# Kernel optimization log

Hardware: AMD Instinct MI355X
Metric: run time of the kernel (lower is better)

## Reference

```python
import jax, jax.numpy as jnp
import numpy as np

B, S, HID = 1, 2048, 2048
H = 16
DN, DR, DV = 128, 64, 128          # qk_nope_head_dim, qk_rope_head_dim, v_head_dim
DQ = DN + DR                        # q_head_dim = 192
QLR, KVLR = 1536, 512               # q_lora_rank, kv_lora_rank
MAXP = 32 * 1024
SCALE = DQ ** -0.5
EPS = 1e-6


def rmsnorm(x, w):
    return x * jax.lax.rsqrt(jnp.mean(x * x, axis=-1, keepdims=True) + EPS) * w


def rotate_half(x):
    h = x.shape[-1] // 2
    return jnp.concatenate((-x[..., h:], x[..., :h]), axis=-1)


def interleave_to_half(x):
    # torch: view(b,h,s,d//2,2).transpose(4,3).reshape(b,h,s,d)
    b, h, s, d = x.shape
    return x.reshape(b, h, s, d // 2, 2).transpose(0, 1, 2, 4, 3).reshape(b, h, s, d)


def setup_inputs() -> dict:
    key = jax.random.key(0)
    ks = jax.random.split(key, 8)
    def w(k, shape):
        fan_in = shape[-1]
        return jax.random.normal(k, shape, jnp.float32) * (fan_in ** -0.5)
    inp = {
        "hidden_states": jax.random.normal(ks[0], (B, S, HID), jnp.float32),
        "q_a_w": w(ks[1], (QLR, HID)),
        "q_a_ln": jnp.ones((QLR,), jnp.float32),
        "q_b_w": w(ks[2], (H * DQ, QLR)),
        "kv_a_w": w(ks[3], (KVLR + DR, HID)),
        "kv_a_ln": jnp.ones((KVLR,), jnp.float32),
        "kv_b_w": w(ks[4], (H * (DN + DV), KVLR)),
        "o_w": w(ks[5], (HID, H * DV)),
    }
    # rotary tables, seq_len = 32k
    inv_freq = 1.0 / (10000.0 ** (np.arange(0, DR, 2, dtype=np.float32) / DR))
    t = np.arange(MAXP, dtype=np.float32)
    freqs = np.outer(t, inv_freq)
    emb = np.concatenate((freqs, freqs), axis=-1)
    inp["cos"] = jnp.asarray(np.cos(emb), jnp.float32)
    inp["sin"] = jnp.asarray(np.sin(emb), jnp.float32)
    # bool mask, True = masked (causal)
    inp["attention_mask"] = jnp.triu(jnp.ones((S, S), bool), 1)[None, None]
    inp["position_ids"] = jnp.arange(S, dtype=jnp.int64 if jax.config.jax_enable_x64 else jnp.int32)[None].repeat(B, 0)
    return inp


def reference(hidden_states, q_a_w, q_a_ln, q_b_w, kv_a_w, kv_a_ln, kv_b_w, o_w,
              cos, sin, attention_mask, position_ids):
    b, s, _ = hidden_states.shape
    # low-rank Q: q_b(LN(q_a(x)))
    q = rmsnorm(hidden_states @ q_a_w.T, q_a_ln) @ q_b_w.T         # [b,s,H*DQ]
    q = q.reshape(b, s, H, DQ).transpose(0, 2, 1, 3)               # [b,H,s,DQ]
    q_nope, q_pe = q[..., :DN], q[..., DN:]
    # compressed KV + decoupled rope key
    ckv = hidden_states @ kv_a_w.T                                  # [b,s,KVLR+DR]
    compressed_kv, k_pe = ckv[..., :KVLR], ckv[..., KVLR:]
    k_pe = k_pe.reshape(b, s, 1, DR).transpose(0, 2, 1, 3)          # [b,1,s,DR]
    kv = rmsnorm(compressed_kv, kv_a_ln) @ kv_b_w.T                 # [b,s,H*(DN+DV)]
    kv = kv.reshape(b, s, H, DN + DV).transpose(0, 2, 1, 3)         # [b,H,s,DN+DV]
    k_nope, value_states = kv[..., :DN], kv[..., DN:]
    # rotary with interleaved->half reorder on the rope slice only
    cos_p = cos[position_ids][:, None]                              # [b,1,s,DR]
    sin_p = sin[position_ids][:, None]
    q_pe = interleave_to_half(q_pe)
    k_pe = interleave_to_half(k_pe)
    q_pe = q_pe * cos_p + rotate_half(q_pe) * sin_p
    k_pe = k_pe * cos_p + rotate_half(k_pe) * sin_p
    query_states = jnp.concatenate((q_nope, q_pe), axis=-1)         # [b,H,s,DQ]
    key_states = jnp.concatenate(
        (k_nope, jnp.broadcast_to(k_pe, (b, H, s, DR))), axis=-1)   # [b,H,s,DQ]
    # manual attention
    scores = jnp.einsum("bhqd,bhkd->bhqk", query_states, key_states) * SCALE
    scores = jnp.where(attention_mask, jnp.float32(-10000.0), scores)
    attn = jax.nn.softmax(scores.astype(jnp.float32), axis=-1).astype(query_states.dtype)
    attn_out = jnp.einsum("bhqk,bhkd->bhqd", attn, value_states)    # [b,H,s,DV]
    attn_out = attn_out.transpose(0, 2, 1, 3).reshape(b, s, H * DV)
    return attn_out @ o_w.T                                         # [b,s,HID]
```

## Files before the change

kernel.cpp:

```cpp
#include <hip/hip_runtime.h>
#include <stdint.h>

typedef unsigned short u16;
typedef __attribute__((ext_vector_type(8))) short short8;
typedef __attribute__((ext_vector_type(4))) float f32x4;
typedef __attribute__((ext_vector_type(4))) unsigned short ushort4_t;
typedef __attribute__((ext_vector_type(4))) float float4_t;

#define DEV_INLINE __device__ __forceinline__

DEV_INLINE u16 f2bf(float f) {
    union { float f; unsigned u; } x; x.f = f;
    unsigned u = x.u;
    unsigned r = (u + 0x7FFFu + ((u >> 16) & 1u)) >> 16;
    return (u16)r;
}

DEV_INLINE float bf2f(u16 b) {
    union { unsigned u; float f; } x; x.u = ((unsigned)b) << 16;
    return x.f;
}

DEV_INLINE float fexp2(float x) {
    float r;
    asm("v_exp_f32 %0, %1" : "=v"(r) : "v"(x));
    return r;
}

DEV_INLINE unsigned cvtpk_bf16(float lo, float hi) {
    unsigned r;
    asm("v_cvt_pk_bf16_f32 %0, %1, %2" : "=v"(r) : "v"(lo), "v"(hi));
    return r;
}

template <int CTRL>
DEV_INLINE float dppmaxf(float x) {
    union { float f; int i; } u; u.f = x;
    int y = __builtin_amdgcn_update_dpp(u.i, u.i, CTRL, 0xf, 0xf, true);
    union { int i; float f; } v; v.i = y;
    return fmaxf(x, v.f);
}

DEV_INLINE float dpp_xor1(float x) {
    union { float f; int i; } u; u.f = x;
    int y = __builtin_amdgcn_update_dpp(u.i, u.i, 0xB1, 0xf, 0xf, true);
    union { int i; float f; } v; v.i = y;
    return v.f;
}

DEV_INLINE float rmax16(float x) {
    x = dppmaxf<0xB1>(x);
    x = dppmaxf<0x4E>(x);
    x = dppmaxf<0x141>(x);
    x = dppmaxf<0x140>(x);
    return x;
}

__global__ void conv_multi(const float* __restrict__ s0, u16* __restrict__ d0, long e0,
                           const float* __restrict__ s1, u16* __restrict__ d1, long e1,
                           const float* __restrict__ s2, u16* __restrict__ d2, long e2,
                           const float* __restrict__ s3, u16* __restrict__ d3, long e3,
                           const float* __restrict__ s4, u16* __restrict__ d4, long e4) {
    long i = (long)blockIdx.x * 256 + threadIdx.x;
    const float* s; u16* d; long base;
    if      (i < e0) { s = s0; d = d0; base = 0; }
    else if (i < e1) { s = s1; d = d1; base = e0; }
    else if (i < e2) { s = s2; d = d2; base = e1; }
    else if (i < e3) { s = s3; d = d3; base = e2; }
    else if (i < e4) { s = s4; d = d4; base = e3; }
    else return;
    long j = i - base;
    float4_t v = ((const float4_t*)s)[j];
    ushort4_t o;
    o.x = f2bf(v.x); o.y = f2bf(v.y); o.z = f2bf(v.z); o.w = f2bf(v.w);
    ((ushort4_t*)d)[j] = o;
}

__global__ void conv_pad(const float* __restrict__ in, u16* __restrict__ out,
                         int rows_valid, long n4, int cols4) {
    long i = (long)blockIdx.x * blockDim.x + threadIdx.x;
    if (i >= n4) return;
    long row = i / cols4;
    ushort4_t o; o.x = 0; o.y = 0; o.z = 0; o.w = 0;
    if (row < rows_valid) {
        float4_t v = ((const float4_t*)in)[i];
        o.x = f2bf(v.x); o.y = f2bf(v.y); o.z = f2bf(v.z); o.w = f2bf(v.w);
    }
    ((ushort4_t*)out)[i] = o;
}

#define BK 32

DEV_INLINE void gload16(const u16* g, u16* l) {
    __builtin_amdgcn_global_load_lds((const __attribute__((address_space(1))) unsigned int*)g,
                                     (__attribute__((address_space(3))) unsigned int*)l,
                                     16, 0, 0);
}

template <typename OT>
__global__ __launch_bounds__(256) void gemm64_db(const u16* __restrict__ A, const u16* __restrict__ B,
                                                 OT* __restrict__ C, int M, int N, int K) {
    __shared__ u16 As[2][64 * BK];
    __shared__ u16 Bs[2][128 * BK];
    const int tid = threadIdx.x;
    const int wid = tid >> 6, lane = tid & 63;
    const int lm = lane & 15, lk = lane >> 4;
    const long bm = (long)blockIdx.y * 64, bn = (long)blockIdx.x * 128;

    f32x4 acc[4][2] = {};

    const int rowS = lane >> 2;
    const int colS = ((lane & 3) ^ ((lane >> 3) & 3)) * 8;
    const int cs = (lm >> 1) & 3;
    const u16* Ag = A + (bm + wid * 16 + rowS) * (long)K + colS;
    const u16* Bg = B + (bn + wid * 32 + rowS) * (long)K + colS;
    const int aoff = wid * 16 * BK;
    const int boff = wid * 32 * BK;

    gload16(Ag, &As[0][aoff]);
    gload16(Bg, &Bs[0][boff]);
    gload16(Bg + 16 * (long)K, &Bs[0][boff + 16 * BK]);
    __syncthreads();

    int cur = 0;
    for (int k0 = 0; k0 < K; k0 += BK) {
        if (k0 + BK < K) {
            gload16(Ag + k0 + BK, &As[cur ^ 1][aoff]);
            gload16(Bg + k0 + BK, &Bs[cur ^ 1][boff]);
            gload16(Bg + 16 * (long)K + k0 + BK, &Bs[cur ^ 1][boff + 16 * BK]);
        }
        short8 af[4], bfr[2];
#pragma unroll
        for (int m = 0; m < 4; ++m)
            af[m] = *(const short8*)&As[cur][(m * 16 + lm) * BK + (lk ^ cs) * 8];
#pragma unroll
        for (int n = 0; n < 2; ++n)
            bfr[n] = *(const short8*)&Bs[cur][(wid * 32 + n * 16 + lm) * BK + (lk ^ cs) * 8];
#pragma unroll
        for (int m = 0; m < 4; ++m)
#pragma unroll
            for (int n = 0; n < 2; ++n)
                acc[m][n] = __builtin_amdgcn_mfma_f32_16x16x32_bf16(af[m], bfr[n], acc[m][n], 0, 0, 0);
        __syncthreads();
        cur ^= 1;
    }

#pragma unroll
    for (int m = 0; m < 4; ++m)
#pragma unroll
        for (int n = 0; n < 2; ++n)
#pragma unroll
            for (int r = 0; r < 4; ++r) {
                long idx = (bm + m * 16 + lk * 4 + r) * (long)N + bn + wid * 32 + n * 16 + lm;
                if constexpr (sizeof(OT) == 4) C[idx] = acc[m][n][r];
                else                           C[idx] = f2bf(acc[m][n][r]);
            }
}

__global__ __launch_bounds__(256) void gemm_qkv(const u16* __restrict__ qnA, const u16* __restrict__ qbB,
                                                const u16* __restrict__ kvnA, const u16* __restrict__ kvbB,
                                                u16* __restrict__ Qb, u16* __restrict__ kvout,
                                                const int* __restrict__ pos,
                                                const float* __restrict__ cosT, const float* __restrict__ sinT) {
    __shared__ u16 As[2][64 * BK];
    __shared__ u16 Bs[2][128 * BK];
    const int tid = threadIdx.x;
    const int wid = tid >> 6, lane = tid & 63;
    const int lm = lane & 15, lk = lane >> 4;

    const bool isq = blockIdx.x < 768;
    const int gx = isq ? blockIdx.x : blockIdx.x - 768;
    const int nb = isq ? 24 : 32;
    const int K  = isq ? 1536 : 512;
    const u16* A = isq ? qnA : kvnA;
    const u16* B = isq ? qbB : kvbB;
    const long bn = (long)(gx % nb) * 128;
    const long bm = (long)(gx / nb) * 64;

    f32x4 acc[4][2] = {};

    const int rowS = lane >> 2;
    const int colS = ((lane & 3) ^ ((lane >> 3) & 3)) * 8;
    const int cs = (lm >> 1) & 3;
    const u16* Ag = A + (bm + wid * 16 + rowS) * (long)K + colS;
    const u16* Bg = B + (bn + wid * 32 + rowS) * (long)K + colS;
    const int aoff = wid * 16 * BK;
    const int boff = wid * 32 * BK;

    gload16(Ag, &As[0][aoff]);
    gload16(Bg, &Bs[0][boff]);
    gload16(Bg + 16 * (long)K, &Bs[0][boff + 16 * BK]);
    __syncthreads();

    int cur = 0;
    for (int k0 = 0; k0 < K; k0 += BK) {
        if (k0 + BK < K) {
            gload16(Ag + k0 + BK, &As[cur ^ 1][aoff]);
            gload16(Bg + k0 + BK, &Bs[cur ^ 1][boff]);
            gload16(Bg + 16 * (long)K + k0 + BK, &Bs[cur ^ 1][boff + 16 * BK]);
        }
        short8 af[4], bfr[2];
#pragma unroll
        for (int m = 0; m < 4; ++m)
            af[m] = *(const short8*)&As[cur][(m * 16 + lm) * BK + (lk ^ cs) * 8];
#pragma unroll
        for (int n = 0; n < 2; ++n)
            bfr[n] = *(const short8*)&Bs[cur][(wid * 32 + n * 16 + lm) * BK + (lk ^ cs) * 8];
#pragma unroll
        for (int m = 0; m < 4; ++m)
#pragma unroll
            for (int n = 0; n < 2; ++n)
                acc[m][n] = __builtin_amdgcn_mfma_f32_16x16x32_bf16(af[m], bfr[n], acc[m][n], 0, 0, 0);
        __syncthreads();
        cur ^= 1;
    }

    if (!isq) {
#pragma unroll
        for (int m = 0; m < 4; ++m)
#pragma unroll
            for (int n = 0; n < 2; ++n)
#pragma unroll
                for (int r = 0; r < 4; ++r) {
                    long idx = (bm + m * 16 + lk * 4 + r) * 4096L + bn + wid * 32 + n * 16 + lm;
                    kvout[idx] = f2bf(acc[m][n][r]);
                }
    } else {
#pragma unroll
        for (int n = 0; n < 2; ++n) {
            const int c = (int)bn + wid * 32 + n * 16 + lm;
            const int h = c / 192;
            const int d = c - h * 192;
            const bool pe = (d >= 128);
            const int t = (d - 128) >> 1;
#pragma unroll
            for (int m = 0; m < 4; ++m)
#pragma unroll
                for (int r = 0; r < 4; ++r) {
                    const long row = bm + m * 16 + lk * 4 + r;
                    float own = acc[m][n][r];
                    float par = dpp_xor1(own);
                    float val = own;
                    if (pe) {
                        long p = pos[row];
                        float cc = cosT[p * 64 + t];
                        float ss = sinT[p * 64 + t];
                        val = (d & 1) ? own * cc + par * ss : own * cc - par * ss;
                    }
                    Qb[((long)h * 2048 + row) * 192 + d] = f2bf(val);
                }
        }
    }
}

__global__ __launch_bounds__(256) void rmsnorm_bf16(const float* __restrict__ in, const float* __restrict__ w,
                                                    u16* __restrict__ out, int ldin, int ldout, int ncols) {
    const int row = blockIdx.x, tid = threadIdx.x;
    const float* x = in + (long)row * ldin;
    float ss = 0.f;
    for (int c = tid; c < ncols; c += 256) { float v = x[c]; ss = fmaf(v, v, ss); }
#pragma unroll
    for (int off = 32; off > 0; off >>= 1) ss += __shfl_down(ss, off);
    __shared__ float part[4];
    if ((tid & 63) == 0) part[tid >> 6] = ss;
    __syncthreads();
    float tot = part[0] + part[1] + part[2] + part[3];
    float rs = rsqrtf(tot / (float)ncols + 1e-6f);
    for (int c = tid; c < ncols; c += 256) out[(long)row * ldout + c] = f2bf(x[c] * rs * w[c]);
}

__global__ void rope_k(const float* __restrict__ ckv, const int* __restrict__ pos,
                       const float* __restrict__ cosT, const float* __restrict__ sinT,
                       u16* __restrict__ Kb) {
    int idx = blockIdx.x * 256 + threadIdx.x;
    if (idx >= 2048 * 32) return;
    int s = idx >> 5, j = idx & 31;
    long p = pos[s];
    const float* row = ckv + (long)s * 2176 + 2048;
    float x0 = row[2 * j], x1 = row[2 * j + 1];
    float c0 = cosT[p * 64 + j], s0 = sinT[p * 64 + j];
    u16 o0 = f2bf(x0 * c0 - x1 * s0);
    u16 o1 = f2bf(x1 * c0 + x0 * s0);
#pragma unroll
    for (int h = 0; h < 16; ++h) {
        u16* kr = Kb + ((long)h * 2048 + s) * 192 + 128;
        kr[2 * j] = o0; kr[2 * j + 1] = o1;
    }
}

__global__ __launch_bounds__(256) void build_kv2(const u16* __restrict__ kv, u16* __restrict__ Kb,
                                                 u16* __restrict__ Vt) {
    __shared__ u16 Ls[128][72];
    const int h = blockIdx.y, s0 = blockIdx.x * 64;
    const int tid = threadIdx.x;
#pragma unroll
    for (int i = 0; i < 8; ++i) {
        int u = i * 256 + tid;
        int r = u >> 5, c8 = (u & 31) * 8;
        short8 x = *(const short8*)(kv + (long)(s0 + r) * 4096 + h * 256 + c8);
        if (c8 < 128) {
            *(short8*)(Kb + ((long)h * 2048 + s0 + r) * 192 + c8) = x;
        } else {
#pragma unroll
            for (int j = 0; j < 8; ++j) {
                int d = c8 - 128 + j;
                Ls[d][r ^ (((d >> 3) & 7) << 3)] = (u16)x[j];
            }
        }
    }
    __syncthreads();
#pragma unroll
    for (int i = 0; i < 8; ++i) {
        int u = i * 256 + tid;
        int d = u >> 4, s4 = (u & 15) * 4;
        int swz = ((d >> 3) & 7) << 3;
        ushort4_t v;
        v.x = Ls[d][(s4 + 0) ^ swz]; v.y = Ls[d][(s4 + 1) ^ swz];
        v.z = Ls[d][(s4 + 2) ^ swz]; v.w = Ls[d][(s4 + 3) ^ swz];
        *(ushort4_t*)(Vt + ((long)h * 128 + d) * 2048 + s0 + s4) = v;
    }
}

__global__ __launch_bounds__(512) void attn_fwd(const u16* __restrict__ Qb, const u16* __restrict__ Kb,
                                                const u16* __restrict__ Vt, u16* __restrict__ Ao) {
    __shared__ __align__(16) char smem[92672];

    const int b = blockIdx.x;
    const int h = (b & 7) * 2 + ((b >> 3) & 1);
    const int pi = b >> 4;
    const int tid = threadIdx.x;
    const int wid = tid >> 6, lane = tid & 63;
    const int lm = lane & 15, lk = lane >> 4;
    const int s = wid >> 2, wp = wid & 3;
    const int t256 = tid & 255;

    u16* Ks0 = (u16*)smem + s * 12288;
    u16* Vs0 = (u16*)(smem + 49152) + s * 8192;
    u16* PsW = (u16*)(smem + 81920) + wid * 640;
    float* ML = (float*)(smem + 92160);
    float* Ob = (float*)smem;

    const u16* Kh = Kb + (long)h * 2048 * 192;
    const u16* Vh = Vt + (long)h * 128 * 2048;

    short8 bones = {};
    if (lm == 0) {
#pragma unroll
        for (int j = 0; j < 8; ++j) bones[j] = (short)0x3F80;
    }
    const float C2 = 0.104117548f;

    for (int half = 0; half < 2; ++half) {
        const int qi = half ? (31 - pi) : pi;
        const int q0 = qi * 64;
        const int nt = 2 * qi + 2;
        const int niter = qi + 1;

        short8 qf[6];
        const u16* qbase = Qb + ((long)h * 2048 + q0 + wp * 16 + lm) * 192;
#pragma unroll
        for (int kf = 0; kf < 6; ++kf) qf[kf] = *(const short8*)(qbase + kf * 32 + lk * 8);

        f32x4 o[8] = {};
        f32x4 o9 = {};
        float mrow[4] = {-1e30f, -1e30f, -1e30f, -1e30f};

        short8 kreg[3], vreg[2];
        {
            const long k0 = s * 32;
#pragma unroll
            for (int i = 0; i < 3; ++i) {
                int idx = i * 256 + t256; int r = idx / 24, c = (idx % 24) * 8;
                kreg[i] = *(const short8*)(Kh + (k0 + r) * 192 + c);
            }
#pragma unroll
            for (int i = 0; i < 2; ++i) {
                int idx = i * 256 + t256; int dv = idx >> 2, kvb = idx & 3;
                vreg[i] = *(const short8*)(Vh + (long)dv * 2048 + k0 + kvb * 8);
            }
#pragma unroll
            for (int i = 0; i < 3; ++i) {
                int idx = i * 256 + t256; int r = idx / 24, c8 = idx % 24;
                *(short8*)&Ks0[r * 192 + ((c8 ^ (r & 7)) << 3)] = kreg[i];
            }
#pragma unroll
            for (int i = 0; i < 2; ++i) {
                int idx = i * 256 + t256; int dv = idx >> 2, kvb = idx & 3;
                *(short8*)&Vs0[kvb * 1024 + ((dv * 8) ^ (kvb * 16))] = vreg[i];
            }
        }
        __syncthreads();

        int cur = 0;
        for (int it = 0; it < niter; ++it) {
            const int ts = 2 * it + s;
            const int k0 = ts * 32;
            const bool more = (it + 1 < niter);

            if (more) {
                const long k0n = (long)(ts + 2) * 32;
#pragma unroll
                for (int i = 0; i < 3; ++i) {
                    int idx = i * 256 + t256; int r = idx / 24, c = (idx % 24) * 8;
                    kreg[i] = *(const short8*)(Kh + (k0n + r) * 192 + c);
                }
#pragma unroll
                for (int i = 0; i < 2; ++i) {
                    int idx = i * 256 + t256; int dv = idx >> 2, kvb = idx & 3;
                    vreg[i] = *(const short8*)(Vh + (long)dv * 2048 + k0n + kvb * 8);
                }
            }

            const u16* KsC = Ks0 + cur * 6144;
            const u16* VsC = Vs0 + cur * 4096;

            f32x4 sfr[2] = {};
#pragma unroll
            for (int n = 0; n < 2; ++n)
#pragma unroll
                for (int kf = 0; kf < 6; ++kf) {
                    short8 kb = *(const short8*)&KsC[(n * 16 + lm) * 192 + (((kf * 4 + lk) ^ (lm & 7)) << 3)];
                    sfr[n] = __builtin_amdgcn_mfma_f32_16x16x32_bf16(qf[kf], kb, sfr[n], 0, 0, 0);
                }

            float sv[2][4];
            const bool bt = (ts >= nt - 2);
#pragma unroll
            for (int n = 0; n < 2; ++n)
#pragma unroll
                for (int r = 0; r < 4; ++r) {
                    float val = sfr[n][r] * C2;
                    if (bt && (k0 + n * 16 + lm > q0 + wp * 16 + lk * 4 + r)) val = -1e30f;
                    sv[n][r] = val;
                }

            float pmax[4];
#pragma unroll
            for (int r = 0; r < 4; ++r)
                pmax[r] = rmax16(fmaxf(sv[0][r], sv[1][r]));
            bool need = (pmax[0] > mrow[0] + 8.f) || (pmax[1] > mrow[1] + 8.f) ||
                        (pmax[2] > mrow[2] + 8.f) || (pmax[3] > mrow[3] + 8.f);
            if (__any(need)) {
#pragma unroll
                for (int r = 0; r < 4; ++r) {
                    float mnew = fmaxf(mrow[r], pmax[r]);
                    float alpha = fexp2(mrow[r] - mnew);
                    mrow[r] = mnew;
#pragma unroll
                    for (int d = 0; d < 8; ++d) o[d][r] *= alpha;
                    o9[r] *= alpha;
                }
            }
#pragma unroll
            for (int n = 0; n < 2; ++n) {
                float p0 = fexp2(sv[n][0] - mrow[0]);
                float p1 = fexp2(sv[n][1] - mrow[1]);
                float p2 = fexp2(sv[n][2] - mrow[2]);
                float p3 = fexp2(sv[n][3] - mrow[3]);
                unsigned pk01 = cvtpk_bf16(p0, p1);
                unsigned pk23 = cvtpk_bf16(p2, p3);
                int rb = (lk * 4) * 40 + n * 16 + lm;
                PsW[rb]       = (u16)pk01;
                PsW[rb + 40]  = (u16)(pk01 >> 16);
                PsW[rb + 80]  = (u16)pk23;
                PsW[rb + 120] = (u16)(pk23 >> 16);
            }

            short8 pf = *(const short8*)&PsW[lm * 40 + lk * 8];
#pragma unroll
            for (int d = 0; d < 8; ++d) {
                short8 vf = *(const short8*)&VsC[lk * 1024 + (((d * 16 + lm) * 8) ^ (lk * 16))];
                o[d] = __builtin_amdgcn_mfma_f32_16x16x32_bf16(pf, vf, o[d], 0, 0, 0);
            }
            o9 = __builtin_amdgcn_mfma_f32_16x16x32_bf16(pf, bones, o9, 0, 0, 0);

            if (more) {
                u16* KsN = Ks0 + (cur ^ 1) * 6144;
                u16* VsN = Vs0 + (cur ^ 1) * 4096;
#pragma unroll
                for (int i = 0; i < 3; ++i) {
                    int idx = i * 256 + t256; int r = idx / 24, c8 = idx % 24;
                    *(short8*)&KsN[r * 192 + ((c8 ^ (r & 7)) << 3)] = kreg[i];
                }
#pragma unroll
                for (int i = 0; i < 2; ++i) {
                    int idx = i * 256 + t256; int dv = idx >> 2, kvb = idx & 3;
                    *(short8*)&VsN[kvb * 1024 + ((dv * 8) ^ (kvb * 16))] = vreg[i];
                }
            }
            __syncthreads();
            cur ^= 1;
        }

        if (s == 1) {
#pragma unroll
            for (int d = 0; d < 8; ++d)
#pragma unroll
                for (int r = 0; r < 4; ++r)
                    Ob[(wp * 16 + lk * 4 + r) * 128 + d * 16 + lm] = o[d][r];
            if (lm == 0) {
#pragma unroll
                for (int r = 0; r < 4; ++r) {
                    int row = wp * 16 + lk * 4 + r;
                    ML[row * 2 + 0] = mrow[r];
                    ML[row * 2 + 1] = o9[r];
                }
            }
        }
        __syncthreads();
        if (s == 0) {
            float e0[4], e1[4], invl[4];
#pragma unroll
            for (int r = 0; r < 4; ++r) {
                int row = wp * 16 + lk * 4 + r;
                float m1 = ML[row * 2 + 0];
                float l1 = ML[row * 2 + 1];
                float l0 = __shfl(o9[r], lane & 48);
                float M = fmaxf(mrow[r], m1);
                e0[r] = fexp2(mrow[r] - M);
                e1[r] = fexp2(m1 - M);
                invl[r] = 1.f / (l0 * e0[r] + l1 * e1[r]);
            }
#pragma unroll
            for (int d = 0; d < 8; ++d)
#pragma unroll
                for (int r = 0; r < 4; ++r) {
                    int row = wp * 16 + lk * 4 + r;
                    float val = (o[d][r] * e0[r] +
                                 Ob[row * 128 + d * 16 + lm] * e1[r]) * invl[r];
                    Ao[((long)q0 + row) * 2048 + h * 128 + d * 16 + lm] = f2bf(val);
                }
        }
        __syncthreads();
    }
}

extern "C" void kernel_launch(void* const* d_in, const int* in_sizes, int n_in,
                              void* d_out, int out_size, void* d_ws, size_t ws_size,
                              hipStream_t stream) {
    (void)in_sizes; (void)n_in; (void)out_size; (void)ws_size;
    const float* hidden  = (const float*)d_in[0];
    const float* q_a_w   = (const float*)d_in[1];
    const float* q_a_ln  = (const float*)d_in[2];
    const float* q_b_w   = (const float*)d_in[3];
    const float* kv_a_w  = (const float*)d_in[4];
    const float* kv_a_ln = (const float*)d_in[5];
    const float* kv_b_w  = (const float*)d_in[6];
    const float* o_w     = (const float*)d_in[7];
    const float* cosT    = (const float*)d_in[8];
    const float* sinT    = (const float*)d_in[9];
    const int*   pos     = (const int*)d_in[11];

    char* ws = (char*)d_ws;
    u16* o_w_bf   = (u16*)(ws + 0);
    u16* qb_w_bf  = (u16*)(ws + 8388608);
    u16* kvb_w_bf = (u16*)(ws + 17825792);
    u16* qn_bf    = (u16*)(ws + 22020096);
    u16* kvn_bf   = (u16*)(ws + 28311552);
    u16* Qb       = (u16*)(ws + 30408704);
    u16* Kb       = (u16*)(ws + 42991616);
    u16* Vt       = (u16*)(ws + 55574528);
    u16* aout_bf  = (u16*)(ws + 63963136);
    u16*   hid_bf    = (u16*)(ws + 72351744);
    u16*   qkva_w_bf = (u16*)(ws + 80740352);
    float* qkva_f    = (float*)(ws + 89653248);
    u16*   kv_f_bf   = (u16*)(ws + 107479040);

    conv_multi<<<17920, 256, 0, stream>>>(
        hidden, hid_bf,    1048576L,
        q_a_w,  qkva_w_bf, 1835008L,
        q_b_w,  qb_w_bf,   3014656L,
        kv_b_w, kvb_w_bf,  3538944L,
        o_w,    o_w_bf,    4587520L);
    conv_pad<<<(640L*2048/4 + 255)/256, 256, 0, stream>>>(kv_a_w, qkva_w_bf + 1536L*2048, 576, 640L*2048/4, 512);

    gemm64_db<float><<<dim3(17, 32), 256, 0, stream>>>(hid_bf, qkva_w_bf, qkva_f, 2048, 2176, 2048);

    rmsnorm_bf16<<<2048, 256, 0, stream>>>(qkva_f, q_a_ln, qn_bf, 2176, 1536, 1536);
    rmsnorm_bf16<<<2048, 256, 0, stream>>>(qkva_f + 1536, kv_a_ln, kvn_bf, 2176, 512, 512);
    rope_k<<<(2048*32)/256, 256, 0, stream>>>(qkva_f, pos, cosT, sinT, Kb);

    gemm_qkv<<<1792, 256, 0, stream>>>(qn_bf, qb_w_bf, kvn_bf, kvb_w_bf, Qb, kv_f_bf, pos, cosT, sinT);

    build_kv2<<<dim3(32, 16), 256, 0, stream>>>(kv_f_bf, Kb, Vt);

    attn_fwd<<<256, 512, 0, stream>>>(Qb, Kb, Vt, aout_bf);

    gemm64_db<float><<<dim3(16, 32), 256, 0, stream>>>(aout_bf, o_w_bf, (float*)d_out, 2048, 2048, 2048);
}
```

Baseline: 235.8 us.

## Fuse launches and write K/V layouts directly from the kv_b GEMM epilogue

Merges the padded kv_a weight conversion into the multi-tensor convert kernel, and merges both RMSNorms and the K rope into one launch. The kv_b GEMM epilogue now writes K_nope straight into the per-head K buffer and transposes V through shared memory into Vt. This removes the intermediate kv buffer and the separate build_kv2 pass. It cuts launch count and one round trip of the KV tensor through global memory, at the cost of a more branchy epilogue with extra barriers in the V tiles.

```diff
diff --git a/kernel.cpp b/kernel.cpp
--- a/kernel.cpp
+++ b/kernel.cpp
@@ -56,37 +56,37 @@
     return x;
 }
 
-__global__ void conv_multi(const float* __restrict__ s0, u16* __restrict__ d0, long e0,
-                           const float* __restrict__ s1, u16* __restrict__ d1, long e1,
-                           const float* __restrict__ s2, u16* __restrict__ d2, long e2,
-                           const float* __restrict__ s3, u16* __restrict__ d3, long e3,
-                           const float* __restrict__ s4, u16* __restrict__ d4, long e4) {
+__global__ void conv_all(const float* __restrict__ s0, u16* __restrict__ d0, long e0,
+                         const float* __restrict__ s1, u16* __restrict__ d1, long e1,
+                         const float* __restrict__ s2, u16* __restrict__ d2, long e2,
+                         const float* __restrict__ s3, u16* __restrict__ d3, long e3,
+                         const float* __restrict__ s4, u16* __restrict__ d4, long e4,
+                         const float* __restrict__ s5, u16* __restrict__ d5, long e5,
+                         int rows_valid, int cols4) {
     long i = (long)blockIdx.x * 256 + threadIdx.x;
+    if (i >= e5) return;
+    if (i >= e4) {
+        long j = i - e4;
+        long row = j / cols4;
+        ushort4_t o; o.x = 0; o.y = 0; o.z = 0; o.w = 0;
+        if (row < rows_valid) {
+            float4_t v = ((const float4_t*)s5)[j];
+            o.x = f2bf(v.x); o.y = f2bf(v.y); o.z = f2bf(v.z); o.w = f2bf(v.w);
+        }
+        ((ushort4_t*)d5)[j] = o;
+        return;
+    }
     const float* s; u16* d; long base;
     if      (i < e0) { s = s0; d = d0; base = 0; }
     else if (i < e1) { s = s1; d = d1; base = e0; }
     else if (i < e2) { s = s2; d = d2; base = e1; }
     else if (i < e3) { s = s3; d = d3; base = e2; }
-    else if (i < e4) { s = s4; d = d4; base = e3; }
-    else return;
+    else             { s = s4; d = d4; base = e3; }
     long j = i - base;
     float4_t v = ((const float4_t*)s)[j];
     ushort4_t o;
     o.x = f2bf(v.x); o.y = f2bf(v.y); o.z = f2bf(v.z); o.w = f2bf(v.w);
     ((ushort4_t*)d)[j] = o;
-}
-
-__global__ void conv_pad(const float* __restrict__ in, u16* __restrict__ out,
-                         int rows_valid, long n4, int cols4) {
-    long i = (long)blockIdx.x * blockDim.x + threadIdx.x;
-    if (i >= n4) return;
-    long row = i / cols4;
-    ushort4_t o; o.x = 0; o.y = 0; o.z = 0; o.w = 0;
-    if (row < rows_valid) {
-        float4_t v = ((const float4_t*)in)[i];
-        o.x = f2bf(v.x); o.y = f2bf(v.y); o.z = f2bf(v.z); o.w = f2bf(v.w);
-    }
-    ((ushort4_t*)out)[i] = o;
 }
 
 #define BK 32
@@ -159,11 +159,12 @@
 
 __global__ __launch_bounds__(256) void gemm_qkv(const u16* __restrict__ qnA, const u16* __restrict__ qbB,
                                                 const u16* __restrict__ kvnA, const u16* __restrict__ kvbB,
-                                                u16* __restrict__ Qb, u16* __restrict__ kvout,
+                                                u16* __restrict__ Qb, u16* __restrict__ Kb, u16* __restrict__ Vt,
                                                 const int* __restrict__ pos,
                                                 const float* __restrict__ cosT, const float* __restrict__ sinT) {
-    __shared__ u16 As[2][64 * BK];
-    __shared__ u16 Bs[2][128 * BK];
+    __shared__ u16 SMEM[12288];
+    u16* As = SMEM;
+    u16* Bs = SMEM + 4096;
     const int tid = threadIdx.x;
     const int wid = tid >> 6, lane = tid & 63;
     const int lm = lane & 15, lk = lane >> 4;
@@ -187,25 +188,25 @@
     const int aoff = wid * 16 * BK;
     const int boff = wid * 32 * BK;
 
-    gload16(Ag, &As[0][aoff]);
-    gload16(Bg, &Bs[0][boff]);
-    gload16(Bg + 16 * (long)K, &Bs[0][boff + 16 * BK]);
+    gload16(Ag, &As[aoff]);
+    gload16(Bg, &Bs[boff]);
+    gload16(Bg + 16 * (long)K, &Bs[boff + 16 * BK]);
     __syncthreads();
 
     int cur = 0;
     for (int k0 = 0; k0 < K; k0 += BK) {
         if (k0 + BK < K) {
-            gload16(Ag + k0 + BK, &As[cur ^ 1][aoff]);
-            gload16(Bg + k0 + BK, &Bs[cur ^ 1][boff]);
-            gload16(Bg + 16 * (long)K + k0 + BK, &Bs[cur ^ 1][boff + 16 * BK]);
+            gload16(Ag + k0 + BK, &As[(cur ^ 1) * 2048 + aoff]);
+            gload16(Bg + k0 + BK, &Bs[(cur ^ 1) * 4096 + boff]);
+            gload16(Bg + 16 * (long)K + k0 + BK, &Bs[(cur ^ 1) * 4096 + boff + 16 * BK]);
         }
         short8 af[4], bfr[2];
 #pragma unroll
         for (int m = 0; m < 4; ++m)
-            af[m] = *(const short8*)&As[cur][(m * 16 + lm) * BK + (lk ^ cs) * 8];
+            af[m] = *(const short8*)&As[cur * 2048 + (m * 16 + lm) * BK + (lk ^ cs) * 8];
 #pragma unroll
         for (int n = 0; n < 2; ++n)
-            bfr[n] = *(const short8*)&Bs[cur][(wid * 32 + n * 16 + lm) * BK + (lk ^ cs) * 8];
+            bfr[n] = *(const short8*)&Bs[cur * 4096 + (wid * 32 + n * 16 + lm) * BK + (lk ^ cs) * 8];
 #pragma unroll
         for (int m = 0; m < 4; ++m)
 #pragma unroll
@@ -215,17 +216,7 @@
         cur ^= 1;
     }
 
-    if (!isq) {
-#pragma unroll
-        for (int m = 0; m < 4; ++m)
-#pragma unroll
-            for (int n = 0; n < 2; ++n)
-#pragma unroll
-                for (int r = 0; r < 4; ++r) {
-                    long idx = (bm + m * 16 + lk * 4 + r) * 4096L + bn + wid * 32 + n * 16 + lm;
-                    kvout[idx] = f2bf(acc[m][n][r]);
-                }
-    } else {
+    if (isq) {
 #pragma unroll
         for (int n = 0; n < 2; ++n) {
             const int c = (int)bn + wid * 32 + n * 16 + lm;
@@ -250,74 +241,88 @@
                     Qb[((long)h * 2048 + row) * 192 + d] = f2bf(val);
                 }
         }
-    }
-}
-
-__global__ __launch_bounds__(256) void rmsnorm_bf16(const float* __restrict__ in, const float* __restrict__ w,
-                                                    u16* __restrict__ out, int ldin, int ldout, int ncols) {
-    const int row = blockIdx.x, tid = threadIdx.x;
-    const float* x = in + (long)row * ldin;
-    float ss = 0.f;
-    for (int c = tid; c < ncols; c += 256) { float v = x[c]; ss = fmaf(v, v, ss); }
-#pragma unroll
-    for (int off = 32; off > 0; off >>= 1) ss += __shfl_down(ss, off);
-    __shared__ float part[4];
-    if ((tid & 63) == 0) part[tid >> 6] = ss;
-    __syncthreads();
-    float tot = part[0] + part[1] + part[2] + part[3];
-    float rs = rsqrtf(tot / (float)ncols + 1e-6f);
-    for (int c = tid; c < ncols; c += 256) out[(long)row * ldout + c] = f2bf(x[c] * rs * w[c]);
-}
-
-__global__ void rope_k(const float* __restrict__ ckv, const int* __restrict__ pos,
-                       const float* __restrict__ cosT, const float* __restrict__ sinT,
-                       u16* __restrict__ Kb) {
-    int idx = blockIdx.x * 256 + threadIdx.x;
-    if (idx >= 2048 * 32) return;
-    int s = idx >> 5, j = idx & 31;
-    long p = pos[s];
-    const float* row = ckv + (long)s * 2176 + 2048;
-    float x0 = row[2 * j], x1 = row[2 * j + 1];
-    float c0 = cosT[p * 64 + j], s0 = sinT[p * 64 + j];
-    u16 o0 = f2bf(x0 * c0 - x1 * s0);
-    u16 o1 = f2bf(x1 * c0 + x0 * s0);
-#pragma unroll
-    for (int h = 0; h < 16; ++h) {
-        u16* kr = Kb + ((long)h * 2048 + s) * 192 + 128;
-        kr[2 * j] = o0; kr[2 * j + 1] = o1;
-    }
-}
-
-__global__ __launch_bounds__(256) void build_kv2(const u16* __restrict__ kv, u16* __restrict__ Kb,
-                                                 u16* __restrict__ Vt) {
-    __shared__ u16 Ls[128][72];
-    const int h = blockIdx.y, s0 = blockIdx.x * 64;
-    const int tid = threadIdx.x;
-#pragma unroll
-    for (int i = 0; i < 8; ++i) {
-        int u = i * 256 + tid;
-        int r = u >> 5, c8 = (u & 31) * 8;
-        short8 x = *(const short8*)(kv + (long)(s0 + r) * 4096 + h * 256 + c8);
-        if (c8 < 128) {
-            *(short8*)(Kb + ((long)h * 2048 + s0 + r) * 192 + c8) = x;
+    } else {
+        const int hh = (gx & 31) >> 1;
+        const bool isV = (gx & 1) != 0;
+        if (!isV) {
+#pragma unroll
+            for (int m = 0; m < 4; ++m)
+#pragma unroll
+                for (int n = 0; n < 2; ++n)
+#pragma unroll
+                    for (int r = 0; r < 4; ++r)
+                        Kb[((long)hh * 2048 + bm + m * 16 + lk * 4 + r) * 192 + wid * 32 + n * 16 + lm]
+                            = f2bf(acc[m][n][r]);
         } else {
-#pragma unroll
-            for (int j = 0; j < 8; ++j) {
-                int d = c8 - 128 + j;
-                Ls[d][r ^ (((d >> 3) & 7) << 3)] = (u16)x[j];
-            }
-        }
-    }
-    __syncthreads();
-#pragma unroll
-    for (int i = 0; i < 8; ++i) {
-        int u = i * 256 + tid;
-        int d = u >> 4, s4 = (u & 15) * 4;
-        int swz = ((d >> 3) & 7) << 3;
-        ushort4_t v;
-        v.x = Ls[d][(s4 + 0) ^ swz]; v.y = Ls[d][(s4 + 1) ^ swz];
-        v.z = Ls[d][(s4 + 2) ^ swz]; v.w = Ls[d][(s4 + 3) ^ swz];
-        *(ushort4_t*)(Vt + ((long)h * 128 + d) * 2048 + s0 + s4) = v;
+            __syncthreads();
+            u16* Ls = SMEM;
+#pragma unroll
+            for (int n = 0; n < 2; ++n) {
+                int d = wid * 32 + n * 16 + lm;
+                int swz = ((d >> 3) & 7) << 3;
+#pragma unroll
+                for (int m = 0; m < 4; ++m)
+#pragma unroll
+                    for (int r = 0; r < 4; ++r) {
+                        int row = m * 16 + lk * 4 + r;
+                        Ls[d * 72 + (row ^ swz)] = f2bf(acc[m][n][r]);
+                    }
+            }
+            __syncthreads();
+#pragma unroll
+            for (int i = 0; i < 8; ++i) {
+                int u = i * 256 + tid;
+                int d = u >> 4, s4 = (u & 15) * 4;
+                int swz = ((d >> 3) & 7) << 3;
+                ushort4_t v;
+                v.x = Ls[d * 72 + ((s4 + 0) ^ swz)]; v.y = Ls[d * 72 + ((s4 + 1) ^ swz)];
+                v.z = Ls[d * 72 + ((s4 + 2) ^ swz)]; v.w = Ls[d * 72 + ((s4 + 3) ^ swz)];
+                *(ushort4_t*)(Vt + ((long)hh * 128 + d) * 2048 + bm + s4) = v;
+            }
+        }
+    }
+}
+
+__global__ __launch_bounds__(256) void norm_rope(const float* __restrict__ qkva,
+                                                 const float* __restrict__ q_ln,
+                                                 const float* __restrict__ kv_ln,
+                                                 u16* __restrict__ qn, u16* __restrict__ kvn,
+                                                 const int* __restrict__ pos,
+                                                 const float* __restrict__ cosT,
+                                                 const float* __restrict__ sinT,
+                                                 u16* __restrict__ Kb) {
+    const int b = blockIdx.x, tid = threadIdx.x;
+    if (b < 4096) {
+        const bool isq = b < 2048;
+        const int row = isq ? b : b - 2048;
+        const int ncols = isq ? 1536 : 512;
+        const float* x = qkva + (long)row * 2176 + (isq ? 0 : 1536);
+        const float* w = isq ? q_ln : kv_ln;
+        u16* out = isq ? (qn + (long)row * 1536) : (kvn + (long)row * 512);
+        float ss = 0.f;
+        for (int c = tid; c < ncols; c += 256) { float v = x[c]; ss = fmaf(v, v, ss); }
+#pragma unroll
+        for (int off = 32; off > 0; off >>= 1) ss += __shfl_down(ss, off);
+        __shared__ float part[4];
+        if ((tid & 63) == 0) part[tid >> 6] = ss;
+        __syncthreads();
+        float tot = part[0] + part[1] + part[2] + part[3];
+        float rs = rsqrtf(tot / (float)ncols + 1e-6f);
+        for (int c = tid; c < ncols; c += 256) out[c] = f2bf(x[c] * rs * w[c]);
+    } else {
+        int idx = (b - 4096) * 256 + tid;
+        int s = idx >> 5, j = idx & 31;
+        long p = pos[s];
+        const float* row = qkva + (long)s * 2176 + 2048;
+        float x0 = row[2 * j], x1 = row[2 * j + 1];
+        float c0 = cosT[p * 64 + j], s0 = sinT[p * 64 + j];
+        u16 o0 = f2bf(x0 * c0 - x1 * s0);
+        u16 o1 = f2bf(x1 * c0 + x0 * s0);
+#pragma unroll
+        for (int h = 0; h < 16; ++h) {
+            u16* kr = Kb + ((long)h * 2048 + s) * 192 + 128;
+            kr[2 * j] = o0; kr[2 * j + 1] = o1;
+        }
     }
 }
 
@@ -564,25 +569,21 @@
     u16*   hid_bf    = (u16*)(ws + 72351744);
     u16*   qkva_w_bf = (u16*)(ws + 80740352);
     float* qkva_f    = (float*)(ws + 89653248);
-    u16*   kv_f_bf   = (u16*)(ws + 107479040);
-
-    conv_multi<<<17920, 256, 0, stream>>>(
-        hidden, hid_bf,    1048576L,
-        q_a_w,  qkva_w_bf, 1835008L,
-        q_b_w,  qb_w_bf,   3014656L,
-        kv_b_w, kvb_w_bf,  3538944L,
-        o_w,    o_w_bf,    4587520L);
-    conv_pad<<<(640L*2048/4 + 255)/256, 256, 0, stream>>>(kv_a_w, qkva_w_bf + 1536L*2048, 576, 640L*2048/4, 512);
+
+    conv_all<<<19200, 256, 0, stream>>>(
+        hidden, hid_bf,                 1048576L,
+        q_a_w,  qkva_w_bf,              1835008L,
+        q_b_w,  qb_w_bf,                3014656L,
+        kv_b_w, kvb_w_bf,               3538944L,
+        o_w,    o_w_bf,                 4587520L,
+        kv_a_w, qkva_w_bf + 1536L*2048, 4915200L,
+        576, 512);
 
     gemm64_db<float><<<dim3(17, 32), 256, 0, stream>>>(hid_bf, qkva_w_bf, qkva_f, 2048, 2176, 2048);
 
-    rmsnorm_bf16<<<2048, 256, 0, stream>>>(qkva_f, q_a_ln, qn_bf, 2176, 1536, 1536);
-    rmsnorm_bf16<<<2048, 256, 0, stream>>>(qkva_f + 1536, kv_a_ln, kvn_bf, 2176, 512, 512);
-    rope_k<<<(2048*32)/256, 256, 0, stream>>>(qkva_f, pos, cosT, sinT, Kb);
-
-    gemm_qkv<<<1792, 256, 0, stream>>>(qn_bf, qb_w_bf, kvn_bf, kvb_w_bf, Qb, kv_f_bf, pos, cosT, sinT);
-
-    build_kv2<<<dim3(32, 16), 256, 0, stream>>>(kv_f_bf, Kb, Vt);
+    norm_rope<<<4352, 256, 0, stream>>>(qkva_f, q_a_ln, kv_a_ln, qn_bf, kvn_bf, pos, cosT, sinT, Kb);
+
+    gemm_qkv<<<1792, 256, 0, stream>>>(qn_bf, qb_w_bf, kvn_bf, kvb_w_bf, Qb, Kb, Vt, pos, cosT, sinT);
 
     attn_fwd<<<256, 512, 0, stream>>>(Qb, Kb, Vt, aout_bf);
 
```

After: 223.2 us. 5.4% less time.
